# Optimization experiments

Hardware: AMD Instinct MI355X
Metric: run time of the kernel (lower is better)

The kernel has to match this reference:

```python
import jax, jax.numpy as jnp
import numpy as np

B, N, C, H = 4, 2048, 2048, 16
DH = C // H  # 128


def setup_inputs() -> dict:
    key = jax.random.key(0)
    ks = jax.random.split(key, 5)
    s = 0.02
    return {
        "x": jax.random.normal(ks[0], (B, N, C), dtype=jnp.float32),
        "w_qkv": jax.random.normal(ks[1], (3 * C, C), dtype=jnp.float32) * s,
        "b_qkv": jax.random.normal(ks[2], (3 * C,), dtype=jnp.float32) * s,
        "w_out": jax.random.normal(ks[3], (C, C), dtype=jnp.float32) * s,
        "b_out": jax.random.normal(ks[4], (C,), dtype=jnp.float32) * s,
    }


def reference(x, w_qkv, b_qkv, w_out, b_out):
    b, n, c = x.shape
    # fused QKV projection (torch Linear: x @ W.T + b)
    qkv = x @ w_qkv.T + b_qkv                      # (B, N, 3C)
    qkv = qkv.reshape(b, n, 3, H, c // H)          # (B, N, 3, H, Dh)
    q, k, v = qkv[:, :, 0], qkv[:, :, 1], qkv[:, :, 2]  # each (B, N, H, Dh)
    # NOTE: faithful to source — no transpose(1,2), so attention mixes HEADS
    # per token: attn has shape (B, N, H, H), scale is 1/sqrt(C).
    attn = jnp.einsum("bnhd,bngd->bnhg", q, k) / jnp.sqrt(jnp.float32(c))
    attn = jax.nn.softmax(attn, axis=-1)
    out = jnp.einsum("bnhg,bngd->bnhd", attn, v)   # (B, N, H, Dh)
    # faithful to source: transpose(1,2) then reshape (interleaves h and n)
    out = out.transpose(0, 2, 1, 3).reshape(b, n, c)
    return out @ w_out.T + b_out
```

## Files before the change

### kernel.cpp

```cpp
#include <hip/hip_runtime.h>

typedef unsigned short u16;
typedef unsigned int u32;
typedef __bf16 bf16x8 __attribute__((ext_vector_type(8)));
typedef float f32x4 __attribute__((ext_vector_type(4)));


__device__ __forceinline__ u16 f2bf(float f) {
    u32 u = __builtin_bit_cast(u32, f);
    u += 0x7FFFu + ((u >> 16) & 1u);
    return (u16)(u >> 16);
}
__device__ __forceinline__ float bf2f(u16 h) {
    return __builtin_bit_cast(float, ((u32)h) << 16);
}

__global__ __launch_bounds__(256) void cvt_bf16(const float* __restrict__ in,
                                                u16* __restrict__ out, int n4) {
    int i = blockIdx.x * 256 + threadIdx.x;
    if (i >= n4) return;
    const float4 f = reinterpret_cast<const float4*>(in)[i];
    ushort4 o;
    o.x = f2bf(f.x); o.y = f2bf(f.y); o.z = f2bf(f.z); o.w = f2bf(f.w);
    reinterpret_cast<ushort4*>(out)[i] = o;
}

typedef const __attribute__((address_space(1))) void* gas1_t;
typedef __attribute__((address_space(3))) void* las3_t;
__device__ __forceinline__ void cp16(const void* g, void* l) {
    __builtin_amdgcn_global_load_lds((gas1_t)g, (las3_t)l, 16, 0, 0);
}

#define BAR()        __builtin_amdgcn_s_barrier()
#define WAIT_LGKM0() asm volatile("s_waitcnt lgkmcnt(0)" ::: "memory")
#define WAIT_VM6()   asm volatile("s_waitcnt vmcnt(6)" ::: "memory")
#define WAIT_VM0()   asm volatile("s_waitcnt vmcnt(0)" ::: "memory")


__device__ __forceinline__ void ld_a4(bf16x8 (&a)[4][2], const char* rdA, int off, int mt0) {
#pragma unroll
    for (int i = 0; i < 4; ++i) {
        a[i][0] = *(const bf16x8*)(rdA + off +        (mt0 + i) * 256);
        a[i][1] = *(const bf16x8*)(rdA + off + 8192 + (mt0 + i) * 256);
    }
}
__device__ __forceinline__ void ld_b2(bf16x8 (&b)[4][2], const char* rdB, int off, int nt0) {
#pragma unroll
    for (int j = 0; j < 2; ++j) {
        b[nt0 + j][0] = *(const bf16x8*)(rdB + off +        (nt0 + j) * 256);
        b[nt0 + j][1] = *(const bf16x8*)(rdB + off + 8192 + (nt0 + j) * 256);
    }
}

template <int MH, int NH>
__device__ __forceinline__ void mfma_quad(f32x4 (&acc)[8][4], bf16x8 (&a)[4][2], bf16x8 (&b)[4][2]) {
    __builtin_amdgcn_s_setprio(1);
#pragma unroll
    for (int ks = 0; ks < 2; ++ks)
#pragma unroll
        for (int i = 0; i < 4; ++i)
#pragma unroll
            for (int j = 0; j < 2; ++j)
                acc[MH * 4 + i][NH * 2 + j] = __builtin_amdgcn_mfma_f32_16x16x32_bf16(
                    a[i][ks], b[NH * 2 + j][ks], acc[MH * 4 + i][NH * 2 + j], 0, 0, 0);
    __builtin_amdgcn_s_setprio(0);
}

template <int OUT_BF16>
__global__ __launch_bounds__(512, 2) void gemm_nt(const u16* __restrict__ A,
                                                  const u16* __restrict__ Bm,
                                                  const float* __restrict__ bias,
                                                  void* __restrict__ Cout,
                                                  int M, int N, int K) {
    __shared__ __align__(16) char lds[131072];

    const int tid  = threadIdx.x;
    const int lane = tid & 63;
    const int wave = tid >> 6;
    const int wm   = wave >> 2;
    const int wn   = wave & 3;
    const int l16  = lane & 15;
    const int kg   = lane >> 4;

    const long bm = (long)blockIdx.y * 256;
    const long bn = (long)blockIdx.x * 256;

    const int srow = tid & 127;
    const int skc  = tid >> 7;
    const u16* gA0 = A  + (bm + srow) * (long)K + skc * 8;
    const u16* gA1 = gA0 + 128 * (long)K;
    const u16* gB0 = Bm + (bn + srow) * (long)K + skc * 8;
    const u16* gB1 = gB0 + 128 * (long)K;
    char* ldst = lds + tid * 16;

#define STAGE_A(HALF, BUF, KT)                                    \
    { const u16* g = ((HALF) ? gA1 : gA0) + (KT) * 64;            \
      char* d = ldst + (BUF) * 32768 + (HALF) * 16384;            \
      cp16(g, d); cp16(g + 32, d + 8192); }
#define STAGE_B(HALF, BUF, KT)                                    \
    { const u16* g = ((HALF) ? gB1 : gB0) + (KT) * 64;            \
      char* d = ldst + 65536 + (BUF) * 32768 + (HALF) * 16384;    \
      cp16(g, d); cp16(g + 32, d + 8192); }

    const char* rdA = lds + wm * 16384 + kg * 2048 + l16 * 16;
    const char* rdB = lds + 65536 + (wn >> 1) * 16384 + kg * 2048
                      + ((wn & 1) * 64 + l16) * 16;

    f32x4 acc[8][4];
#pragma unroll
    for (int i = 0; i < 8; ++i)
#pragma unroll
        for (int j = 0; j < 4; ++j)
#pragma unroll
            for (int r = 0; r < 4; ++r) acc[i][j][r] = 0.f;

    const int NT = K >> 6;

    STAGE_B(0, 0, 0); STAGE_B(1, 0, 0); STAGE_A(0, 0, 0); STAGE_A(1, 0, 0);
    STAGE_B(0, 1, 1); STAGE_B(1, 1, 1); STAGE_A(0, 1, 1);
    WAIT_VM6();
    BAR();

    bf16x8 a[4][2], b[4][2];

#define KTILE(RBUF, A1B, A1K, BB, BKT, A0B, A0K)                  \
    {                                                             \
        const int ro = (RBUF) * 32768;                            \
                                     \
        ld_a4(a, rdA, ro, 0);                                     \
        ld_b2(b, rdB, ro, 0);                                     \
        STAGE_A(1, A1B, A1K);                                     \
        BAR(); WAIT_LGKM0();                                      \
        mfma_quad<0, 0>(acc, a, b);                               \
        BAR();                                                    \
                                     \
        ld_b2(b, rdB, ro, 2);                                     \
        BAR(); WAIT_LGKM0();                                      \
        mfma_quad<0, 1>(acc, a, b);                               \
        BAR();                                                    \
                                     \
        ld_a4(a, rdA, ro, 4);                                     \
        STAGE_B(0, BB, BKT); STAGE_B(1, BB, BKT);                 \
        BAR(); WAIT_LGKM0();                                      \
        mfma_quad<1, 0>(acc, a, b);                               \
        BAR();                                                    \
                                     \
        STAGE_A(0, A0B, A0K);                                     \
        BAR(); WAIT_LGKM0();                                      \
        mfma_quad<1, 1>(acc, a, b);                               \
        WAIT_VM6();                                               \
        BAR();                                                    \
    }

    const int NIT = NT >> 1;
    for (int it = 0; it < NIT; ++it) {
        const int T = 2 * it;
        int t2 = T + 2; if (t2 >= NT) t2 -= NT;
        int t3 = T + 3; if (t3 >= NT) t3 -= NT;
        KTILE(0, 1, T + 1, 0, t2, 0, t2);
        KTILE(1, 0, t2,    1, t3, 1, t3);
    }
#undef KTILE
#undef STAGE_A
#undef STAGE_B

    WAIT_VM0();

    const long crow0 = bm + wm * 128;
    const long ccol0 = bn + wn * 64 + l16;
#pragma unroll
    for (int nt = 0; nt < 4; ++nt) {
        const long col = ccol0 + nt * 16;
        const float bc = bias[col];
#pragma unroll
        for (int mt = 0; mt < 8; ++mt) {
#pragma unroll
            for (int r = 0; r < 4; ++r) {
                const long row = crow0 + mt * 16 + kg * 4 + r;
                float v = acc[mt][nt][r] + bc;
                if (OUT_BF16)
                    ((u16*)Cout)[row * (long)N + col] = f2bf(v);
                else
                    ((float*)Cout)[row * (long)N + col] = v;
            }
        }
    }
}

__global__ __launch_bounds__(256) void attn(const u16* __restrict__ qkv,
                                            u16* __restrict__ outb) {
    __shared__ float sQ[16 * 132];
    __shared__ float sK[16 * 132];
    __shared__ float sV[16 * 132];
    __shared__ float sP[16 * 17];

    const int tid = threadIdx.x;
    const int token = blockIdx.x;
    const int b = token >> 11;
    const int n = token & 2047;
    const u16* row = qkv + (long)token * 6144;

    {
        const int r  = tid >> 4;
        const int c8 = (tid & 15) * 8;
#pragma unroll
        for (int m = 0; m < 3; ++m) {
            const uint4 u = *reinterpret_cast<const uint4*>(row + m * 2048 + tid * 8);
            float* dst = (m == 0 ? sQ : (m == 1 ? sK : sV)) + r * 132 + c8;
            float4 lo, hi;
            lo.x = bf2f((u16)u.x); lo.y = bf2f((u16)(u.x >> 16));
            lo.z = bf2f((u16)u.y); lo.w = bf2f((u16)(u.y >> 16));
            hi.x = bf2f((u16)u.z); hi.y = bf2f((u16)(u.z >> 16));
            hi.z = bf2f((u16)u.w); hi.w = bf2f((u16)(u.w >> 16));
            *reinterpret_cast<float4*>(dst)     = lo;
            *reinterpret_cast<float4*>(dst + 4) = hi;
        }
    }
    __syncthreads();

    {
        const int h = tid >> 4, g = tid & 15;
        const float4* qr = reinterpret_cast<const float4*>(&sQ[h * 132]);
        const float4* kr = reinterpret_cast<const float4*>(&sK[g * 132]);
        float s = 0.f;
#pragma unroll
        for (int d = 0; d < 32; ++d) {
            const float4 a = qr[d], k4 = kr[d];
            s += a.x * k4.x + a.y * k4.y + a.z * k4.z + a.w * k4.w;
        }
        s *= 0.022097086912079608f;
        float mx = s;
#pragma unroll
        for (int o = 8; o >= 1; o >>= 1) mx = fmaxf(mx, __shfl_xor(mx, o, 16));
        const float e = __expf(s - mx);
        float sum = e;
#pragma unroll
        for (int o = 8; o >= 1; o >>= 1) sum += __shfl_xor(sum, o, 16);
        sP[h * 17 + g] = e / sum;
    }
    __syncthreads();

    {
        const int h = tid >> 4, dblk = tid & 15;
        float p[16];
#pragma unroll
        for (int g = 0; g < 16; ++g) p[g] = sP[h * 17 + g];
        float4 o0 = {0.f, 0.f, 0.f, 0.f}, o1 = {0.f, 0.f, 0.f, 0.f};
#pragma unroll
        for (int g = 0; g < 16; ++g) {
            const float* vr = &sV[g * 132 + dblk * 8];
            const float4 v0 = *reinterpret_cast<const float4*>(vr);
            const float4 v1 = *reinterpret_cast<const float4*>(vr + 4);
            o0.x += p[g] * v0.x; o0.y += p[g] * v0.y; o0.z += p[g] * v0.z; o0.w += p[g] * v0.w;
            o1.x += p[g] * v1.x; o1.y += p[g] * v1.y; o1.z += p[g] * v1.z; o1.w += p[g] * v1.w;
        }
        const long rr = (long)h * 128 + (n >> 4);
        const long cc = (long)(n & 15) * 128 + dblk * 8;
        u16* dst = outb + ((long)b * 2048 + rr) * 2048 + cc;
        uint4 pk;
        pk.x = (u32)f2bf(o0.x) | ((u32)f2bf(o0.y) << 16);
        pk.y = (u32)f2bf(o0.z) | ((u32)f2bf(o0.w) << 16);
        pk.z = (u32)f2bf(o1.x) | ((u32)f2bf(o1.y) << 16);
        pk.w = (u32)f2bf(o1.z) | ((u32)f2bf(o1.w) << 16);
        *reinterpret_cast<uint4*>(dst) = pk;
    }
}

extern "C" void kernel_launch(void* const* d_in, const int* in_sizes, int n_in,
                              void* d_out, int out_size, void* d_ws, size_t ws_size,
                              hipStream_t stream) {
    const float* x     = (const float*)d_in[0];
    const float* w_qkv = (const float*)d_in[1];
    const float* b_qkv = (const float*)d_in[2];
    const float* w_out = (const float*)d_in[3];
    const float* b_out = (const float*)d_in[4];
    float* out = (float*)d_out;

    char* ws = (char*)d_ws;
    u16* xb    = (u16*)(ws);
    u16* wqkvb = (u16*)(ws + 33554432);
    u16* woutb = (u16*)(ws + 58720256);
    u16* qkvb  = (u16*)(ws + 67108864);
    u16* attnb = xb;

    cvt_bf16<<<16384, 256, 0, stream>>>(x,     xb,    16777216 / 4);
    cvt_bf16<<<12288, 256, 0, stream>>>(w_qkv, wqkvb, 12582912 / 4);
    cvt_bf16<<<4096,  256, 0, stream>>>(w_out, woutb, 4194304 / 4);

    dim3 g1(24, 32);
    gemm_nt<1><<<g1, 512, 0, stream>>>(xb, wqkvb, b_qkv, qkvb, 8192, 6144, 2048);

    attn<<<8192, 256, 0, stream>>>(qkvb, attnb);

    dim3 g2(8, 32);
    gemm_nt<0><<<g2, 512, 0, stream>>>(attnb, woutb, b_out, out, 8192, 2048, 2048);
}
```

Before: 540.1 us.

## Software-pipeline LDS fragment loads with MFMA using double-buffered register fragments

New measurement: 556.6 us. 3.1% more time.

```diff
diff --git a/kernel.cpp b/kernel.cpp
--- a/kernel.cpp
+++ b/kernel.cpp
@@ -32,37 +32,30 @@
 }
 
 #define BAR()        __builtin_amdgcn_s_barrier()
-#define WAIT_LGKM0() asm volatile("s_waitcnt lgkmcnt(0)" ::: "memory")
-#define WAIT_VM6()   asm volatile("s_waitcnt vmcnt(6)" ::: "memory")
-#define WAIT_VM0()   asm volatile("s_waitcnt vmcnt(0)" ::: "memory")
-
-
-__device__ __forceinline__ void ld_a4(bf16x8 (&a)[4][2], const char* rdA, int off, int mt0) {
-#pragma unroll
-    for (int i = 0; i < 4; ++i) {
-        a[i][0] = *(const bf16x8*)(rdA + off +        (mt0 + i) * 256);
-        a[i][1] = *(const bf16x8*)(rdA + off + 8192 + (mt0 + i) * 256);
-    }
-}
-__device__ __forceinline__ void ld_b2(bf16x8 (&b)[4][2], const char* rdB, int off, int nt0) {
-#pragma unroll
-    for (int j = 0; j < 2; ++j) {
-        b[nt0 + j][0] = *(const bf16x8*)(rdB + off +        (nt0 + j) * 256);
-        b[nt0 + j][1] = *(const bf16x8*)(rdB + off + 8192 + (nt0 + j) * 256);
-    }
-}
-
-template <int MH, int NH>
-__device__ __forceinline__ void mfma_quad(f32x4 (&acc)[8][4], bf16x8 (&a)[4][2], bf16x8 (&b)[4][2]) {
+#define SBAR0()      __builtin_amdgcn_sched_barrier(0)
+#define WAIT_LGKM(n) asm volatile("s_waitcnt lgkmcnt(" #n ")" ::: "memory")
+#define WAIT_VM(n)   asm volatile("s_waitcnt vmcnt(" #n ")" ::: "memory")
+
+
+__device__ __forceinline__ void ld_a(bf16x8 (&d)[4], const char* rdA, int off, int mt0) {
+#pragma unroll
+    for (int i = 0; i < 4; ++i)
+        d[i] = *(const bf16x8*)(rdA + off + (mt0 + i) * 256);
+}
+__device__ __forceinline__ void ld_b(bf16x8 (&d)[4], const char* rdB, int off) {
+#pragma unroll
+    for (int j = 0; j < 4; ++j)
+        d[j] = *(const bf16x8*)(rdB + off + j * 256);
+}
+
+template <int R0>
+__device__ __forceinline__ void mfma16(f32x4 (&acc)[8][4], bf16x8 (&a)[4], bf16x8 (&b)[4]) {
     __builtin_amdgcn_s_setprio(1);
 #pragma unroll
-    for (int ks = 0; ks < 2; ++ks)
-#pragma unroll
-        for (int i = 0; i < 4; ++i)
-#pragma unroll
-            for (int j = 0; j < 2; ++j)
-                acc[MH * 4 + i][NH * 2 + j] = __builtin_amdgcn_mfma_f32_16x16x32_bf16(
-                    a[i][ks], b[NH * 2 + j][ks], acc[MH * 4 + i][NH * 2 + j], 0, 0, 0);
+    for (int i = 0; i < 4; ++i)
+#pragma unroll
+        for (int j = 0; j < 4; ++j)
+            acc[R0 + i][j] = __builtin_amdgcn_mfma_f32_16x16x32_bf16(a[i], b[j], acc[R0 + i][j], 0, 0, 0);
     __builtin_amdgcn_s_setprio(0);
 }
 
@@ -117,39 +110,40 @@
     const int NT = K >> 6;
 
     STAGE_B(0, 0, 0); STAGE_B(1, 0, 0); STAGE_A(0, 0, 0); STAGE_A(1, 0, 0);
-    STAGE_B(0, 1, 1); STAGE_B(1, 1, 1); STAGE_A(0, 1, 1);
-    WAIT_VM6();
+    STAGE_B(0, 1, 1); STAGE_B(1, 1, 1); STAGE_A(0, 1, 1); STAGE_A(1, 1, 1);
+    WAIT_VM(8);
     BAR();
 
-    bf16x8 a[4][2], b[4][2];
-
-#define KTILE(RBUF, A1B, A1K, BB, BKT, A0B, A0K)                  \
+    bf16x8 aC[4], aN[4], bC[4], bN[4];
+    ld_b(bC, rdB, 0);
+    ld_a(aC, rdA, 0, 0);
+
+#define KTILE(RB, NB, BKT, AKT)                                   \
     {                                                             \
-        const int ro = (RBUF) * 32768;                            \
-                                     \
-        ld_a4(a, rdA, ro, 0);                                     \
-        ld_b2(b, rdB, ro, 0);                                     \
-        STAGE_A(1, A1B, A1K);                                     \
-        BAR(); WAIT_LGKM0();                                      \
-        mfma_quad<0, 0>(acc, a, b);                               \
-        BAR();                                                    \
-                                     \
-        ld_b2(b, rdB, ro, 2);                                     \
-        BAR(); WAIT_LGKM0();                                      \
-        mfma_quad<0, 1>(acc, a, b);                               \
-        BAR();                                                    \
-                                     \
-        ld_a4(a, rdA, ro, 4);                                     \
-        STAGE_B(0, BB, BKT); STAGE_B(1, BB, BKT);                 \
-        BAR(); WAIT_LGKM0();                                      \
-        mfma_quad<1, 0>(acc, a, b);                               \
-        BAR();                                                    \
-                                     \
-        STAGE_A(0, A0B, A0K);                                     \
-        BAR(); WAIT_LGKM0();                                      \
-        mfma_quad<1, 1>(acc, a, b);                               \
-        WAIT_VM6();                                               \
-        BAR();                                                    \
+        constexpr int ro = (RB) * 32768;                          \
+        constexpr int rn = (NB) * 32768;                          \
+                           \
+        ld_a(aN, rdA, ro, 4);                                     \
+        SBAR0();                                                  \
+        mfma16<0>(acc, aC, bC);                                   \
+                           \
+        ld_b(bN, rdB, ro + 8192);    \
+        ld_a(aC, rdA, ro + 8192, 0);                              \
+        SBAR0();                                                  \
+        mfma16<4>(acc, aN, bC);                                   \
+        WAIT_LGKM(4); BAR();                                      \
+                           \
+        ld_a(aN, rdA, ro + 8192, 4);                              \
+        STAGE_B(0, RB, BKT); STAGE_B(1, RB, BKT);                 \
+        SBAR0();                                                  \
+        mfma16<0>(acc, aC, bN);                                   \
+        WAIT_LGKM(0); WAIT_VM(4); BAR();                          \
+         \
+        ld_b(bC, rdB, rn);                                        \
+        ld_a(aC, rdA, rn, 0);                                     \
+        STAGE_A(0, RB, AKT); STAGE_A(1, RB, AKT);                 \
+        SBAR0();                                                  \
+        mfma16<4>(acc, aN, bN);                                   \
     }
 
     const int NIT = NT >> 1;
@@ -157,14 +151,14 @@
         const int T = 2 * it;
         int t2 = T + 2; if (t2 >= NT) t2 -= NT;
         int t3 = T + 3; if (t3 >= NT) t3 -= NT;
-        KTILE(0, 1, T + 1, 0, t2, 0, t2);
-        KTILE(1, 0, t2,    1, t3, 1, t3);
+        KTILE(0, 1, t2, t2);
+        KTILE(1, 0, t3, t3);
     }
 #undef KTILE
 #undef STAGE_A
 #undef STAGE_B
 
-    WAIT_VM0();
+    WAIT_VM(0);
 
     const long crow0 = bm + wm * 128;
     const long ccol0 = bn + wn * 64 + l16;
```

## Switch GEMM to 32x32x16 MFMA with row-major XOR-swizzled LDS layout

Applied to the files above, without the earlier changes.

New measurement: 470.8 us. 12.8% less time.

```diff
diff --git a/kernel.cpp b/kernel.cpp
--- a/kernel.cpp
+++ b/kernel.cpp
@@ -3,7 +3,7 @@
 typedef unsigned short u16;
 typedef unsigned int u32;
 typedef __bf16 bf16x8 __attribute__((ext_vector_type(8)));
-typedef float f32x4 __attribute__((ext_vector_type(4)));
+typedef float f32x16 __attribute__((ext_vector_type(16)));
 
 
 __device__ __forceinline__ u16 f2bf(float f) {
@@ -37,32 +37,31 @@
 #define WAIT_VM0()   asm volatile("s_waitcnt vmcnt(0)" ::: "memory")
 
 
-__device__ __forceinline__ void ld_a4(bf16x8 (&a)[4][2], const char* rdA, int off, int mt0) {
-#pragma unroll
-    for (int i = 0; i < 4; ++i) {
-        a[i][0] = *(const bf16x8*)(rdA + off +        (mt0 + i) * 256);
-        a[i][1] = *(const bf16x8*)(rdA + off + 8192 + (mt0 + i) * 256);
-    }
-}
-__device__ __forceinline__ void ld_b2(bf16x8 (&b)[4][2], const char* rdB, int off, int nt0) {
-#pragma unroll
-    for (int j = 0; j < 2; ++j) {
-        b[nt0 + j][0] = *(const bf16x8*)(rdB + off +        (nt0 + j) * 256);
-        b[nt0 + j][1] = *(const bf16x8*)(rdB + off + 8192 + (nt0 + j) * 256);
-    }
+__device__ __forceinline__ void ld_a2(bf16x8 (&a)[2][4], const char* base,
+                                      const int (&o)[4], int mt0) {
+#pragma unroll
+    for (int m = 0; m < 2; ++m)
+#pragma unroll
+        for (int ks = 0; ks < 4; ++ks)
+            a[m][ks] = *(const bf16x8*)(base + (mt0 + m) * 4096 + o[ks]);
+}
+__device__ __forceinline__ void ld_b4(bf16x8 (&bb)[4], const char* base,
+                                      const int (&o)[4], int nt) {
+#pragma unroll
+    for (int ks = 0; ks < 4; ++ks)
+        bb[ks] = *(const bf16x8*)(base + nt * 4096 + o[ks]);
 }
 
 template <int MH, int NH>
-__device__ __forceinline__ void mfma_quad(f32x4 (&acc)[8][4], bf16x8 (&a)[4][2], bf16x8 (&b)[4][2]) {
+__device__ __forceinline__ void quad(f32x16 (&acc)[4][2], bf16x8 (&a)[2][4],
+                                     bf16x8 (&b)[2][4]) {
     __builtin_amdgcn_s_setprio(1);
 #pragma unroll
-    for (int ks = 0; ks < 2; ++ks)
-#pragma unroll
-        for (int i = 0; i < 4; ++i)
-#pragma unroll
-            for (int j = 0; j < 2; ++j)
-                acc[MH * 4 + i][NH * 2 + j] = __builtin_amdgcn_mfma_f32_16x16x32_bf16(
-                    a[i][ks], b[NH * 2 + j][ks], acc[MH * 4 + i][NH * 2 + j], 0, 0, 0);
+    for (int ks = 0; ks < 4; ++ks)
+#pragma unroll
+        for (int m = 0; m < 2; ++m)
+            acc[MH * 2 + m][NH] = __builtin_amdgcn_mfma_f32_32x32x16_bf16(
+                a[m][ks], b[NH][ks], acc[MH * 2 + m][NH], 0, 0, 0);
     __builtin_amdgcn_s_setprio(0);
 }
 
@@ -79,40 +78,44 @@
     const int wave = tid >> 6;
     const int wm   = wave >> 2;
     const int wn   = wave & 3;
-    const int l16  = lane & 15;
-    const int kg   = lane >> 4;
+    const int r32  = lane & 31;
+    const int half = lane >> 5;
 
     const long bm = (long)blockIdx.y * 256;
     const long bn = (long)blockIdx.x * 256;
 
-    const int srow = tid & 127;
-    const int skc  = tid >> 7;
+    const int srow = tid >> 3;
+    const int skc  = ((tid & 7) - srow) & 7;
     const u16* gA0 = A  + (bm + srow) * (long)K + skc * 8;
     const u16* gA1 = gA0 + 128 * (long)K;
     const u16* gB0 = Bm + (bn + srow) * (long)K + skc * 8;
     const u16* gB1 = gB0 + 128 * (long)K;
+    const long hK  = 64 * (long)K;
     char* ldst = lds + tid * 16;
 
 #define STAGE_A(HALF, BUF, KT)                                    \
     { const u16* g = ((HALF) ? gA1 : gA0) + (KT) * 64;            \
       char* d = ldst + (BUF) * 32768 + (HALF) * 16384;            \
-      cp16(g, d); cp16(g + 32, d + 8192); }
+      cp16(g, d); cp16(g + hK, d + 8192); }
 #define STAGE_B(HALF, BUF, KT)                                    \
     { const u16* g = ((HALF) ? gB1 : gB0) + (KT) * 64;            \
       char* d = ldst + 65536 + (BUF) * 32768 + (HALF) * 16384;    \
-      cp16(g, d); cp16(g + 32, d + 8192); }
-
-    const char* rdA = lds + wm * 16384 + kg * 2048 + l16 * 16;
-    const char* rdB = lds + 65536 + (wn >> 1) * 16384 + kg * 2048
-                      + ((wn & 1) * 64 + l16) * 16;
-
-    f32x4 acc[8][4];
-#pragma unroll
-    for (int i = 0; i < 8; ++i)
-#pragma unroll
-        for (int j = 0; j < 4; ++j)
-#pragma unroll
-            for (int r = 0; r < 4; ++r) acc[i][j][r] = 0.f;
+      cp16(g, d); cp16(g + hK, d + 8192); }
+
+    const char* rdA = lds + wm * 16384 + r32 * 128;
+    const char* rdB = lds + 65536 + (wn >> 1) * 16384 + ((wn & 1) * 64 + r32) * 128;
+    const int c = (half + r32) & 7;
+    int o[4];
+#pragma unroll
+    for (int ks = 0; ks < 4; ++ks) o[ks] = ((c + 2 * ks) & 7) << 4;
+
+    f32x16 acc[4][2];
+#pragma unroll
+    for (int i = 0; i < 4; ++i)
+#pragma unroll
+        for (int j = 0; j < 2; ++j)
+#pragma unroll
+            for (int r = 0; r < 16; ++r) acc[i][j][r] = 0.f;
 
     const int NT = K >> 6;
 
@@ -121,33 +124,34 @@
     WAIT_VM6();
     BAR();
 
-    bf16x8 a[4][2], b[4][2];
-
-#define KTILE(RBUF, A1B, A1K, BB, BKT, A0B, A0K)                  \
+    bf16x8 a[2][4], b[2][4];
+
+#define KTILE(RB, A1B, A1K, BB, BKT, A0B, A0K)                    \
     {                                                             \
-        const int ro = (RBUF) * 32768;                            \
-                                     \
-        ld_a4(a, rdA, ro, 0);                                     \
-        ld_b2(b, rdB, ro, 0);                                     \
+        const char* rA = rdA + (RB) * 32768;                      \
+        const char* rB = rdB + (RB) * 32768;                      \
+                                                 \
+        ld_a2(a, rA, o, 0);                                       \
+        ld_b4(b[0], rB, o, 0);                                    \
         STAGE_A(1, A1B, A1K);                                     \
         BAR(); WAIT_LGKM0();                                      \
-        mfma_quad<0, 0>(acc, a, b);                               \
+        quad<0, 0>(acc, a, b);                                    \
         BAR();                                                    \
-                                     \
-        ld_b2(b, rdB, ro, 2);                                     \
+                                                 \
+        ld_b4(b[1], rB, o, 1);                                    \
         BAR(); WAIT_LGKM0();                                      \
-        mfma_quad<0, 1>(acc, a, b);                               \
+        quad<0, 1>(acc, a, b);                                    \
         BAR();                                                    \
-                                     \
-        ld_a4(a, rdA, ro, 4);                                     \
+                                                 \
+        ld_a2(a, rA, o, 2);                                       \
         STAGE_B(0, BB, BKT); STAGE_B(1, BB, BKT);                 \
         BAR(); WAIT_LGKM0();                                      \
-        mfma_quad<1, 0>(acc, a, b);                               \
+        quad<1, 0>(acc, a, b);                                    \
         BAR();                                                    \
-                                     \
+                                                 \
         STAGE_A(0, A0B, A0K);                                     \
         BAR(); WAIT_LGKM0();                                      \
-        mfma_quad<1, 1>(acc, a, b);                               \
+        quad<1, 1>(acc, a, b);                                    \
         WAIT_VM6();                                               \
         BAR();                                                    \
     }
@@ -167,17 +171,17 @@
     WAIT_VM0();
 
     const long crow0 = bm + wm * 128;
-    const long ccol0 = bn + wn * 64 + l16;
-#pragma unroll
-    for (int nt = 0; nt < 4; ++nt) {
-        const long col = ccol0 + nt * 16;
+    const long ccol0 = bn + wn * 64;
+#pragma unroll
+    for (int nt = 0; nt < 2; ++nt) {
+        const long col = ccol0 + nt * 32 + r32;
         const float bc = bias[col];
 #pragma unroll
-        for (int mt = 0; mt < 8; ++mt) {
-#pragma unroll
-            for (int r = 0; r < 4; ++r) {
-                const long row = crow0 + mt * 16 + kg * 4 + r;
-                float v = acc[mt][nt][r] + bc;
+        for (int mt = 0; mt < 4; ++mt) {
+#pragma unroll
+            for (int reg = 0; reg < 16; ++reg) {
+                const long row = crow0 + mt * 32 + (reg & 3) + 8 * (reg >> 2) + 4 * half;
+                float v = acc[mt][nt][reg] + bc;
                 if (OUT_BF16)
                     ((u16*)Cout)[row * (long)N + col] = f2bf(v);
                 else
```
